# Kernel tuning notes

Hardware: AMD Instinct MI355X
Metric: run time of the kernel (lower is better)

## Reference

```python
import jax, jax.numpy as jnp
import numpy as np

THRESHOLD_IOU = 0.8  # forward default in the original module


def setup_inputs() -> dict:
    key = jax.random.key(0)
    k1, k2, k3, k4 = jax.random.split(key, 4)
    N = M = 16
    H = W = 768
    # Binary masks (the original zeroes pixels to 0.0 and tests >0 via torch.where)
    masks_a = (jax.random.uniform(k1, (N, H, W)) > 0.6).astype(jnp.float32)
    masks_b = (jax.random.uniform(k2, (M, H, W)) > 0.6).astype(jnp.float32)
    # Make a few masks identical across labels so the IoU>threshold (suppression)
    # branch is exercised, not just the partial-overlap zeroing branch.
    masks_b = masks_b.at[:4].set(masks_a[:4])
    scores_a = jax.random.uniform(k3, (N,))
    scores_b = jax.random.uniform(k4, (M,))
    return {"masks_a": masks_a, "masks_b": masks_b,
            "scores_a": scores_a, "scores_b": scores_b}


def _overlap_filter(masks_a, masks_b, scores_a, scores_b, thr):
    # Sequential pairwise IoU + overlap zeroing, faithful to the original
    # nested product(enumerate(masks), enumerate(other_masks)) loop order
    # (i outer, j inner), where each pair sees masks already modified by
    # earlier pairs. Pruning ("keep") is applied after the loop; here it is
    # represented with static shapes as keep flags + zeroed-out rows.
    N, H, W = masks_a.shape
    M = masks_b.shape[0]
    P = H * W
    A0 = masks_a.reshape(N, P)
    B0 = masks_b.reshape(M, P)

    def body(carry, k):
        A, B, fi, fj = carry
        i = k // M
        j = k % M
        a = A[i]  # [P]
        b = B[j]  # [P]
        abin = a > 0
        bbin = b > 0
        inter = abin & bbin
        inter_sum = jnp.sum(inter.astype(jnp.float32))
        union_sum = jnp.sum((abin | bbin).astype(jnp.float32))
        iou = inter_sum / jnp.maximum(union_sum, 1.0)
        a_wins = scores_a[i] > scores_b[j]
        suppress = iou > thr                 # mark whole loser mask for removal
        zero_case = (iou > 0) & ~suppress    # zero overlapped pixels of loser
        b_new = jnp.where(zero_case & a_wins & inter, 0.0, b)
        a_new = jnp.where(zero_case & (~a_wins) & inter, 0.0, a)
        A = A.at[i].set(a_new)
        B = B.at[j].set(b_new)
        fj = fj.at[j].set(fj[j] | (suppress & a_wins))
        fi = fi.at[i].set(fi[i] | (suppress & ~a_wins))
        return (A, B, fi, fj), None

    fi0 = jnp.zeros(N, dtype=bool)
    fj0 = jnp.zeros(M, dtype=bool)
    (A, B, fi, fj), _ = jax.lax.scan(body, (A0, B0, fi0, fj0), jnp.arange(N * M))
    keep_a = ~fi
    keep_b = ~fj
    A = jnp.where(keep_a[:, None], A, 0.0)
    B = jnp.where(keep_b[:, None], B, 0.0)
    return A.reshape(N, H, W), B.reshape(M, H, W), keep_a, keep_b


def reference(masks_a, masks_b, scores_a, scores_b):
    return _overlap_filter(masks_a, masks_b, scores_a, scores_b, THRESHOLD_IOU)
```

## Files before the change

### kernel.cpp

```cpp
#include <hip/hip_runtime.h>
#include <stdint.h>

#define NM 16
#define HW_P 589824
#define U8PM 9216
#define C4PM 4608
#define F4PM 147456
#define F4PT 2359296
#define PT 512
#define NG 8
#define EWG 64

typedef unsigned long long u64;
typedef float vf4 __attribute__((ext_vector_type(4)));


__device__ __forceinline__ unsigned aload(const unsigned* p) {
    return __hip_atomic_load(p, __ATOMIC_RELAXED, __HIP_MEMORY_SCOPE_AGENT);
}
__device__ __forceinline__ void astore(unsigned* p, unsigned v) {
    __hip_atomic_store(p, v, __ATOMIC_RELAXED, __HIP_MEMORY_SCOPE_AGENT);
}
__device__ __forceinline__ unsigned afadd(unsigned* p, unsigned v) {
    return __hip_atomic_fetch_add(p, v, __ATOMIC_RELAXED, __HIP_MEMORY_SCOPE_AGENT);
}
__device__ __forceinline__ u64 aload64(const u64* p) {
    return __hip_atomic_load(p, __ATOMIC_RELAXED, __HIP_MEMORY_SCOPE_AGENT);
}

__device__ __forceinline__ uint32_t spread4(uint32_t x) {
    uint32_t t = (x | (x << 12)) & 0x000F000Fu;
    t = (t | (t << 6)) & 0x03030303u;
    t = (t | (t << 3)) & 0x11111111u;
    return t;
}

__global__ __launch_bounds__(256) void binarize_kernel(
    const float* __restrict__ ma, const float* __restrict__ mb,
    uint32_t* __restrict__ bitsA, uint32_t* __restrict__ bitsB,
    uint4* __restrict__ meta4)
{
    if (blockIdx.x == 0) {
        uint4 z; z.x = z.y = z.z = z.w = 0u;
        meta4[threadIdx.x] = z;
    }
    int g = blockIdx.x * 256 + threadIdx.x;
    int tensor = (g >= F4PT);
    int lg = tensor ? (g - F4PT) : g;
    const float* src = tensor ? mb : ma;
    vf4 v = __builtin_nontemporal_load(((const vf4*)src) + lg);
    u64 q0 = __ballot(v.x > 0.0f);
    u64 q1 = __ballot(v.y > 0.0f);
    u64 q2 = __ballot(v.z > 0.0f);
    u64 q3 = __ballot(v.w > 0.0f);
    int lane = threadIdx.x & 63;
    if (lane < 8) {
        uint32_t wd = spread4((uint32_t)(q0 >> (8 * lane)) & 0xFFu)
                    | (spread4((uint32_t)(q1 >> (8 * lane)) & 0xFFu) << 1)
                    | (spread4((uint32_t)(q2 >> (8 * lane)) & 0xFFu) << 2)
                    | (spread4((uint32_t)(q3 >> (8 * lane)) & 0xFFu) << 3);
        uint32_t* bits = tensor ? bitsB : bitsA;
        bits[((lg & ~63) >> 3) + lane] = wd;
    }
}

__global__ __launch_bounds__(PT, 1) void pipeline_kernel(
    const float* __restrict__ sa, const float* __restrict__ sb,
    uint32_t* bitsA, uint32_t* bitsB, unsigned* meta, u64* msg)
{
    unsigned* cnt    = meta;
    unsigned* winner = meta + 8;
    int* flagsA      = (int*)(meta + 16);
    int* flagsB      = (int*)(meta + 32);
    unsigned* consF  = meta + 48;
    unsigned* prodF  = meta + 80;

    const int tid = threadIdx.x;
    const int wave = tid >> 6, lane = tid & 63;

    __shared__ int s_g;
    __shared__ int4 part[8];

    if (tid == 0) {
        int xcc;
        asm volatile("s_getreg_b32 %0, hwreg(HW_REG_XCC_ID)" : "=s"(xcc));
        xcc &= 7;
        unsigned slot = afadd(&cnt[xcc], 1u);
        int mine = -1;
        if (slot < NG) {
            if (slot == NG - 1) {
                unsigned exp = 0u;
                __hip_atomic_compare_exchange_strong(
                    winner, &exp, (unsigned)(xcc + 1),
                    __ATOMIC_RELAXED, __ATOMIC_RELAXED, __HIP_MEMORY_SCOPE_AGENT);
            }
            unsigned w;
            while (!(w = aload(winner))) __builtin_amdgcn_s_sleep(1);
            if (w == (unsigned)(xcc + 1)) mine = (int)slot;
        }
        s_g = mine;
    }
    __syncthreads();
    const int g = s_g;
    if (g < 0) return;

    const int c0 = 2 * g, c1 = 2 * g + 1;
    uint4* A4 = (uint4*)bitsA;
    uint4* B4 = (uint4*)bitsB;

    u64 b0[18], b1[18];

    int v0 = 0, v1 = 0;
#pragma unroll
    for (int w = 0; w < 9; ++w) {
        uint4 q0 = B4[(size_t)c0 * C4PM + tid + PT * w];
        uint4 q1 = B4[(size_t)c1 * C4PM + tid + PT * w];
        b0[2 * w] = ((u64)q0.y << 32) | q0.x; b0[2 * w + 1] = ((u64)q0.w << 32) | q0.z;
        b1[2 * w] = ((u64)q1.y << 32) | q1.x; b1[2 * w + 1] = ((u64)q1.w << 32) | q1.z;
        v0 += __popcll(b0[2 * w]) + __popcll(b0[2 * w + 1]);
        v1 += __popcll(b1[2 * w]) + __popcll(b1[2 * w + 1]);
    }
#pragma unroll
    for (int off = 32; off >= 1; off >>= 1) {
        v0 += __shfl_xor(v0, off); v1 += __shfl_xor(v1, off);
    }
    if (lane == 0) { int4 p; p.x = v0; p.y = v1; p.z = 0; p.w = 0; part[wave] = p; }
    __syncthreads();
    int pcb0 = 0, pcb1 = 0;
#pragma unroll
    for (int w = 0; w < 8; ++w) { pcb0 += part[w].x; pcb1 += part[w].y; }
    float sb0 = sb[c0], sb1 = sb[c1];
    int fb0 = 0, fb1 = 0;
    __syncthreads();

    for (int t = 0; t < NM; ++t) {
        int pca, fa;
        u64 a[18];

        if (g == 0) {
            pca = 0; fa = 0;
#pragma unroll
            for (int w = 0; w < 9; ++w) {
                uint4 q = A4[(size_t)t * C4PM + tid + PT * w];
                a[2 * w] = ((u64)q.y << 32) | q.x;
                a[2 * w + 1] = ((u64)q.w << 32) | q.z;
            }
        } else {
            const unsigned* fptr = &prodF[((g - 1) * 16 + t) * 4];
            unsigned v;
            do { v = aload(fptr); } while (!v);
            asm volatile("" ::: "memory");
            pca = (int)((v >> 1) & 0xFFFFFu);
            fa  = (int)((v >> 21) & 1u);
            const u64* slot_in = msg + (size_t)((g - 1) * 4 + (t & 3)) * U8PM;
#pragma unroll
            for (int w = 0; w < 9; ++w) {
                int base2 = 2 * tid + 1024 * w;
                a[2 * w]     = aload64(&slot_in[base2]);
                a[2 * w + 1] = aload64(&slot_in[base2 + 1]);
            }
        }

        int i0 = 0, i1 = 0, itr = 0, ipc = 0;
#pragma unroll
        for (int w = 0; w < 18; ++w) {
            u64 ab0 = a[w] & b0[w];
            i0 += __popcll(ab0);
            i1 += __popcll(a[w] & b1[w]);
            itr += __popcll(ab0 & b1[w]);
        }
        if (g == 0) {
#pragma unroll
            for (int w = 0; w < 18; ++w) ipc += __popcll(a[w]);
        }
#pragma unroll
        for (int off = 32; off >= 1; off >>= 1) {
            i0 += __shfl_xor(i0, off); i1 += __shfl_xor(i1, off);
            itr += __shfl_xor(itr, off); ipc += __shfl_xor(ipc, off);
        }
        if (lane == 0) {
            int4 p; p.x = i0; p.y = i1; p.z = itr; p.w = ipc; part[wave] = p;
        }
        __syncthreads();
        if (g > 0 && tid == 65)
            astore(&consF[(g - 1) * 4], (unsigned)(t + 1));
        int I0 = 0, I1 = 0, T = 0, PC = 0;
#pragma unroll
        for (int w = 0; w < 8; ++w) {
            int4 p = part[w];
            I0 += p.x; I1 += p.y; T += p.z; PC += p.w;
        }
        if (g == 0) pca = PC;

        float sai = sa[t];
        bool aupd = false;
        {
            int inter = I0;
            int uni = pca + pcb0 - inter;
            float iou = (float)inter / fmaxf((float)uni, 1.0f);
            bool aw = sai > sb0;
            if (iou > 0.8f) { if (aw) fb0 = 1; else fa = 1; }
            else if (inter > 0) {
                if (aw) {
                    pcb0 -= inter;
#pragma unroll
                    for (int w = 0; w < 18; ++w) b0[w] &= ~a[w];
                } else {
                    pca -= inter; aupd = true;
#pragma unroll
                    for (int w = 0; w < 18; ++w) a[w] &= ~b0[w];
                }
            }
        }
        {
            int inter = aupd ? (I1 - T) : I1;
            int uni = pca + pcb1 - inter;
            float iou = (float)inter / fmaxf((float)uni, 1.0f);
            bool aw = sai > sb1;
            if (iou > 0.8f) { if (aw) fb1 = 1; else fa = 1; }
            else if (inter > 0) {
                if (aw) {
                    pcb1 -= inter;
#pragma unroll
                    for (int w = 0; w < 18; ++w) b1[w] &= ~a[w];
                } else {
                    pca -= inter;
#pragma unroll
                    for (int w = 0; w < 18; ++w) a[w] &= ~b1[w];
                }
            }
        }

        if (g < NG - 1) {
            if (t >= 4) {
                const unsigned* cp = &consF[g * 4];
                while (aload(cp) < (unsigned)(t - 3)) {}
                asm volatile("" ::: "memory");
            }
            uint4* so = (uint4*)(msg + (size_t)(g * 4 + (t & 3)) * U8PM);
#pragma unroll
            for (int w = 0; w < 9; ++w) {
                uint4 q;
                q.x = (uint32_t)a[2 * w];     q.y = (uint32_t)(a[2 * w] >> 32);
                q.z = (uint32_t)a[2 * w + 1]; q.w = (uint32_t)(a[2 * w + 1] >> 32);
                so[tid + PT * w] = q;
            }
            __syncthreads();
            if (tid == 0)
                astore(&prodF[(g * 16 + t) * 4],
                       1u | ((unsigned)pca << 1) | ((unsigned)fa << 21));
        } else {
            uint4* Ar = A4 + (size_t)t * C4PM;
#pragma unroll
            for (int w = 0; w < 9; ++w) {
                uint4 q;
                q.x = (uint32_t)a[2 * w];     q.y = (uint32_t)(a[2 * w] >> 32);
                q.z = (uint32_t)a[2 * w + 1]; q.w = (uint32_t)(a[2 * w + 1] >> 32);
                Ar[tid + PT * w] = q;
            }
            if (tid == 0) flagsA[t] = fa;
            __syncthreads();
        }
    }

    uint4* Wc0 = B4 + (size_t)c0 * C4PM;
    uint4* Wc1 = B4 + (size_t)c1 * C4PM;
#pragma unroll
    for (int w = 0; w < 9; ++w) {
        uint4 q0, q1;
        q0.x = (uint32_t)b0[2 * w];     q0.y = (uint32_t)(b0[2 * w] >> 32);
        q0.z = (uint32_t)b0[2 * w + 1]; q0.w = (uint32_t)(b0[2 * w + 1] >> 32);
        q1.x = (uint32_t)b1[2 * w];     q1.y = (uint32_t)(b1[2 * w] >> 32);
        q1.z = (uint32_t)b1[2 * w + 1]; q1.w = (uint32_t)(b1[2 * w + 1] >> 32);
        Wc0[tid + PT * w] = q0;
        Wc1[tid + PT * w] = q1;
    }
    if (tid == 0) { flagsB[c0] = fb0; flagsB[c1] = fb1; }
}

__global__ __launch_bounds__(256) void expand_kernel(
    const uint32_t* __restrict__ bitsA, const uint32_t* __restrict__ bitsB,
    const int* __restrict__ meta, float* __restrict__ out)
{
    int g = blockIdx.x * 256 + threadIdx.x;
    int tensor = (g >= F4PT);
    int lg = tensor ? (g - F4PT) : g;
    const uint32_t* bits = tensor ? bitsB : bitsA;
    const int* flags = meta + (tensor ? 32 : 16);
    int m = lg / F4PM;
    bool keep = (flags[m] == 0);
    uint32_t wd = keep ? bits[lg >> 3] : 0u;
    int sh = (lg & 7) * 4;
    vf4 o;
    o.x = ((wd >> (sh + 0)) & 1u) ? 1.0f : 0.0f;
    o.y = ((wd >> (sh + 1)) & 1u) ? 1.0f : 0.0f;
    o.z = ((wd >> (sh + 2)) & 1u) ? 1.0f : 0.0f;
    o.w = ((wd >> (sh + 3)) & 1u) ? 1.0f : 0.0f;
    __builtin_nontemporal_store(o, ((vf4*)out) + g);
    if (g < 2 * NM) {
        out[(size_t)2 * NM * HW_P + g] = meta[16 + g] ? 0.0f : 1.0f;
    }
}

extern "C" void kernel_launch(void* const* d_in, const int* in_sizes, int n_in,
                              void* d_out, int out_size, void* d_ws, size_t ws_size,
                              hipStream_t stream)
{
    const float* ma = (const float*)d_in[0];
    const float* mb = (const float*)d_in[1];
    const float* sa = (const float*)d_in[2];
    const float* sb = (const float*)d_in[3];
    float* out = (float*)d_out;
    char* ws = (char*)d_ws;

    uint32_t* bitsA = (uint32_t*)(ws);
    uint32_t* bitsB = (uint32_t*)(ws + 1179648);
    unsigned* meta  = (unsigned*)(ws + 2359296);
    u64* msg        = (u64*)(ws + 2363392);

    binarize_kernel<<<18432, 256, 0, stream>>>(ma, mb, bitsA, bitsB,
                                               (uint4*)meta);
    pipeline_kernel<<<EWG, PT, 0, stream>>>(sa, sb, bitsA, bitsB, meta, msg);
    expand_kernel<<<18432, 256, 0, stream>>>(bitsA, bitsB, (const int*)meta, out);
}
```

Before: 226.8 us.

## Split each pipeline stage across two workgroups exchanging half-mask partial counts

Each of the eight pipeline stages is now split over two workgroups, each handling half of the pixel range, so the launch needs 16 co-resident workgroups on one XCC instead of 8. Partner workgroups swap their partial intersection and popcount sums every step through agent-scope atomic slots tagged with the step number, and the message buffers now carry half-masks. This halves per-workgroup register data and per-step memory traffic to shorten the serial critical path, but it adds a cross-workgroup handshake on every step and more spin-waiting.

```diff
diff --git a/kernel.cpp b/kernel.cpp
--- a/kernel.cpp
+++ b/kernel.cpp
@@ -4,12 +4,13 @@
 #define NM 16
 #define HW_P 589824
 #define U8PM 9216
-#define C4PM 4608
+#define U8PH 4608
 #define F4PM 147456
 #define F4PT 2359296
 #define PT 512
 #define NG 8
-#define EWG 64
+#define NW 16
+#define EWG 128
 
 typedef unsigned long long u64;
 typedef float vf4 __attribute__((ext_vector_type(4)));
@@ -26,6 +27,9 @@
 }
 __device__ __forceinline__ u64 aload64(const u64* p) {
     return __hip_atomic_load(p, __ATOMIC_RELAXED, __HIP_MEMORY_SCOPE_AGENT);
+}
+__device__ __forceinline__ void astore64(u64* p, u64 v) {
+    __hip_atomic_store(p, v, __ATOMIC_RELAXED, __HIP_MEMORY_SCOPE_AGENT);
 }
 
 __device__ __forceinline__ uint32_t spread4(uint32_t x) {
@@ -43,6 +47,7 @@
     if (blockIdx.x == 0) {
         uint4 z; z.x = z.y = z.z = z.w = 0u;
         meta4[threadIdx.x] = z;
+        meta4[threadIdx.x + 256] = z;
     }
     int g = blockIdx.x * 256 + threadIdx.x;
     int tensor = (g >= F4PT);
@@ -73,12 +78,13 @@
     int* flagsA      = (int*)(meta + 16);
     int* flagsB      = (int*)(meta + 32);
     unsigned* consF  = meta + 48;
-    unsigned* prodF  = meta + 80;
+    unsigned* prodF  = meta + 112;
+    u64* xchg        = (u64*)(meta + 1024);
 
     const int tid = threadIdx.x;
     const int wave = tid >> 6, lane = tid & 63;
 
-    __shared__ int s_g;
+    __shared__ int s_slot;
     __shared__ int4 part[8];
 
     if (tid == 0) {
@@ -87,8 +93,8 @@
         xcc &= 7;
         unsigned slot = afadd(&cnt[xcc], 1u);
         int mine = -1;
-        if (slot < NG) {
-            if (slot == NG - 1) {
+        if (slot < NW) {
+            if (slot == NW - 1) {
                 unsigned exp = 0u;
                 __hip_atomic_compare_exchange_strong(
                     winner, &exp, (unsigned)(xcc + 1),
@@ -98,72 +104,103 @@
             while (!(w = aload(winner))) __builtin_amdgcn_s_sleep(1);
             if (w == (unsigned)(xcc + 1)) mine = (int)slot;
         }
-        s_g = mine;
+        s_slot = mine;
     }
     __syncthreads();
-    const int g = s_g;
-    if (g < 0) return;
+    const int sl = s_slot;
+    if (sl < 0) return;
+    const int g = sl >> 1, h = sl & 1;
+    const int ch = g * 2 + h;
+    const int inch = (g - 1) * 2 + h;
+
+    u64* A8 = (u64*)bitsA;
+    u64* B8 = (u64*)bitsB;
+
+    auto load9 = [&](const u64* base, u64* dst) {
+        const uint4* b4 = (const uint4*)base;
+#pragma unroll
+        for (int w = 0; w < 4; ++w) {
+            uint4 q = b4[tid + PT * w];
+            dst[2 * w]     = ((u64)q.y << 32) | q.x;
+            dst[2 * w + 1] = ((u64)q.w << 32) | q.z;
+        }
+        dst[8] = base[4096 + tid];
+    };
+    auto load9_agent = [&](const u64* base, u64* dst) {
+#pragma unroll
+        for (int w = 0; w < 4; ++w) {
+            int i2 = 2 * tid + 1024 * w;
+            dst[2 * w]     = aload64(&base[i2]);
+            dst[2 * w + 1] = aload64(&base[i2 + 1]);
+        }
+        dst[8] = aload64(&base[4096 + tid]);
+    };
+    auto store9 = [&](u64* base, const u64* src) {
+        uint4* b4 = (uint4*)base;
+#pragma unroll
+        for (int w = 0; w < 4; ++w) {
+            uint4 q;
+            q.x = (uint32_t)src[2 * w];     q.y = (uint32_t)(src[2 * w] >> 32);
+            q.z = (uint32_t)src[2 * w + 1]; q.w = (uint32_t)(src[2 * w + 1] >> 32);
+            b4[tid + PT * w] = q;
+        }
+        base[4096 + tid] = src[8];
+    };
 
     const int c0 = 2 * g, c1 = 2 * g + 1;
-    uint4* A4 = (uint4*)bitsA;
-    uint4* B4 = (uint4*)bitsB;
-
-    u64 b0[18], b1[18];
-
+    u64 b0[9], b1[9];
+    load9(B8 + (size_t)c0 * U8PM + (size_t)h * U8PH, b0);
+    load9(B8 + (size_t)c1 * U8PM + (size_t)h * U8PH, b1);
     int v0 = 0, v1 = 0;
 #pragma unroll
-    for (int w = 0; w < 9; ++w) {
-        uint4 q0 = B4[(size_t)c0 * C4PM + tid + PT * w];
-        uint4 q1 = B4[(size_t)c1 * C4PM + tid + PT * w];
-        b0[2 * w] = ((u64)q0.y << 32) | q0.x; b0[2 * w + 1] = ((u64)q0.w << 32) | q0.z;
-        b1[2 * w] = ((u64)q1.y << 32) | q1.x; b1[2 * w + 1] = ((u64)q1.w << 32) | q1.z;
-        v0 += __popcll(b0[2 * w]) + __popcll(b0[2 * w + 1]);
-        v1 += __popcll(b1[2 * w]) + __popcll(b1[2 * w + 1]);
-    }
+    for (int w = 0; w < 9; ++w) { v0 += __popcll(b0[w]); v1 += __popcll(b1[w]); }
 #pragma unroll
     for (int off = 32; off >= 1; off >>= 1) {
         v0 += __shfl_xor(v0, off); v1 += __shfl_xor(v1, off);
     }
     if (lane == 0) { int4 p; p.x = v0; p.y = v1; p.z = 0; p.w = 0; part[wave] = p; }
     __syncthreads();
-    int pcb0 = 0, pcb1 = 0;
-#pragma unroll
-    for (int w = 0; w < 8; ++w) { pcb0 += part[w].x; pcb1 += part[w].y; }
+    int pcb0h = 0, pcb1h = 0;
+#pragma unroll
+    for (int w = 0; w < 8; ++w) { pcb0h += part[w].x; pcb1h += part[w].y; }
+    __syncthreads();
+
+    {
+        u64* myx = xchg + (size_t)(ch * 2 + 1) * 2;
+        if (tid == 0)
+            astore64(&myx[0], (u64)pcb0h | ((u64)pcb1h << 20) | (1ull << 40));
+    }
+    int pcb0, pcb1;
+    {
+        const u64* px = xchg + (size_t)((g * 2 + (1 - h)) * 2 + 1) * 2;
+        u64 x0;
+        do { x0 = aload64(&px[0]); } while ((unsigned)(x0 >> 40) != 1u);
+        pcb0 = pcb0h + (int)(x0 & 0xFFFFF);
+        pcb1 = pcb1h + (int)((x0 >> 20) & 0xFFFFF);
+    }
     float sb0 = sb[c0], sb1 = sb[c1];
     int fb0 = 0, fb1 = 0;
-    __syncthreads();
 
     for (int t = 0; t < NM; ++t) {
         int pca, fa;
-        u64 a[18];
+        u64 a[9];
 
         if (g == 0) {
+            load9(A8 + (size_t)t * U8PM + (size_t)h * U8PH, a);
             pca = 0; fa = 0;
-#pragma unroll
-            for (int w = 0; w < 9; ++w) {
-                uint4 q = A4[(size_t)t * C4PM + tid + PT * w];
-                a[2 * w] = ((u64)q.y << 32) | q.x;
-                a[2 * w + 1] = ((u64)q.w << 32) | q.z;
-            }
         } else {
-            const unsigned* fptr = &prodF[((g - 1) * 16 + t) * 4];
+            const unsigned* fptr = &prodF[(inch * 16 + t) * 4];
             unsigned v;
             do { v = aload(fptr); } while (!v);
             asm volatile("" ::: "memory");
             pca = (int)((v >> 1) & 0xFFFFFu);
             fa  = (int)((v >> 21) & 1u);
-            const u64* slot_in = msg + (size_t)((g - 1) * 4 + (t & 3)) * U8PM;
-#pragma unroll
-            for (int w = 0; w < 9; ++w) {
-                int base2 = 2 * tid + 1024 * w;
-                a[2 * w]     = aload64(&slot_in[base2]);
-                a[2 * w + 1] = aload64(&slot_in[base2 + 1]);
-            }
+            load9_agent(msg + (size_t)(inch * 4 + (t & 3)) * U8PH, a);
         }
 
         int i0 = 0, i1 = 0, itr = 0, ipc = 0;
 #pragma unroll
-        for (int w = 0; w < 18; ++w) {
+        for (int w = 0; w < 9; ++w) {
             u64 ab0 = a[w] & b0[w];
             i0 += __popcll(ab0);
             i1 += __popcll(a[w] & b1[w]);
@@ -171,7 +208,7 @@
         }
         if (g == 0) {
 #pragma unroll
-            for (int w = 0; w < 18; ++w) ipc += __popcll(a[w]);
+            for (int w = 0; w < 9; ++w) ipc += __popcll(a[w]);
         }
 #pragma unroll
         for (int off = 32; off >= 1; off >>= 1) {
@@ -183,12 +220,32 @@
         }
         __syncthreads();
         if (g > 0 && tid == 65)
-            astore(&consF[(g - 1) * 4], (unsigned)(t + 1));
-        int I0 = 0, I1 = 0, T = 0, PC = 0;
+            astore(&consF[inch * 4], (unsigned)(t + 1));
+        int I0h = 0, I1h = 0, Th = 0, PCh = 0;
 #pragma unroll
         for (int w = 0; w < 8; ++w) {
             int4 p = part[w];
-            I0 += p.x; I1 += p.y; T += p.z; PC += p.w;
+            I0h += p.x; I1h += p.y; Th += p.z; PCh += p.w;
+        }
+
+        unsigned tg = (unsigned)(t + 2);
+        {
+            u64* myx = xchg + (size_t)(ch * 2 + (t & 1)) * 2;
+            if (tid == 0) {
+                astore64(&myx[0], (u64)I0h | ((u64)I1h << 20) | ((u64)tg << 40));
+                astore64(&myx[1], (u64)Th  | ((u64)PCh << 20) | ((u64)tg << 40));
+            }
+        }
+        int I0, I1, T, PC;
+        {
+            const u64* px = xchg + (size_t)((g * 2 + (1 - h)) * 2 + (t & 1)) * 2;
+            u64 x0, x1;
+            do { x0 = aload64(&px[0]); } while ((unsigned)(x0 >> 40) != tg);
+            do { x1 = aload64(&px[1]); } while ((unsigned)(x1 >> 40) != tg);
+            I0 = I0h + (int)(x0 & 0xFFFFF);
+            I1 = I1h + (int)((x0 >> 20) & 0xFFFFF);
+            T  = Th  + (int)(x1 & 0xFFFFF);
+            PC = PCh + (int)((x1 >> 20) & 0xFFFFF);
         }
         if (g == 0) pca = PC;
 
@@ -204,11 +261,11 @@
                 if (aw) {
                     pcb0 -= inter;
 #pragma unroll
-                    for (int w = 0; w < 18; ++w) b0[w] &= ~a[w];
+                    for (int w = 0; w < 9; ++w) b0[w] &= ~a[w];
                 } else {
                     pca -= inter; aupd = true;
 #pragma unroll
-                    for (int w = 0; w < 18; ++w) a[w] &= ~b0[w];
+                    for (int w = 0; w < 9; ++w) a[w] &= ~b0[w];
                 }
             }
         }
@@ -222,60 +279,36 @@
                 if (aw) {
                     pcb1 -= inter;
 #pragma unroll
-                    for (int w = 0; w < 18; ++w) b1[w] &= ~a[w];
+                    for (int w = 0; w < 9; ++w) b1[w] &= ~a[w];
                 } else {
                     pca -= inter;
 #pragma unroll
-                    for (int w = 0; w < 18; ++w) a[w] &= ~b1[w];
+                    for (int w = 0; w < 9; ++w) a[w] &= ~b1[w];
                 }
             }
         }
 
         if (g < NG - 1) {
             if (t >= 4) {
-                const unsigned* cp = &consF[g * 4];
+                const unsigned* cp = &consF[ch * 4];
                 while (aload(cp) < (unsigned)(t - 3)) {}
                 asm volatile("" ::: "memory");
             }
-            uint4* so = (uint4*)(msg + (size_t)(g * 4 + (t & 3)) * U8PM);
-#pragma unroll
-            for (int w = 0; w < 9; ++w) {
-                uint4 q;
-                q.x = (uint32_t)a[2 * w];     q.y = (uint32_t)(a[2 * w] >> 32);
-                q.z = (uint32_t)a[2 * w + 1]; q.w = (uint32_t)(a[2 * w + 1] >> 32);
-                so[tid + PT * w] = q;
-            }
+            store9(msg + (size_t)(ch * 4 + (t & 3)) * U8PH, a);
             __syncthreads();
             if (tid == 0)
-                astore(&prodF[(g * 16 + t) * 4],
+                astore(&prodF[(ch * 16 + t) * 4],
                        1u | ((unsigned)pca << 1) | ((unsigned)fa << 21));
         } else {
-            uint4* Ar = A4 + (size_t)t * C4PM;
-#pragma unroll
-            for (int w = 0; w < 9; ++w) {
-                uint4 q;
-                q.x = (uint32_t)a[2 * w];     q.y = (uint32_t)(a[2 * w] >> 32);
-                q.z = (uint32_t)a[2 * w + 1]; q.w = (uint32_t)(a[2 * w + 1] >> 32);
-                Ar[tid + PT * w] = q;
-            }
-            if (tid == 0) flagsA[t] = fa;
+            store9(A8 + (size_t)t * U8PM + (size_t)h * U8PH, a);
+            if (h == 0 && tid == 0) flagsA[t] = fa;
             __syncthreads();
         }
     }
 
-    uint4* Wc0 = B4 + (size_t)c0 * C4PM;
-    uint4* Wc1 = B4 + (size_t)c1 * C4PM;
-#pragma unroll
-    for (int w = 0; w < 9; ++w) {
-        uint4 q0, q1;
-        q0.x = (uint32_t)b0[2 * w];     q0.y = (uint32_t)(b0[2 * w] >> 32);
-        q0.z = (uint32_t)b0[2 * w + 1]; q0.w = (uint32_t)(b0[2 * w + 1] >> 32);
-        q1.x = (uint32_t)b1[2 * w];     q1.y = (uint32_t)(b1[2 * w] >> 32);
-        q1.z = (uint32_t)b1[2 * w + 1]; q1.w = (uint32_t)(b1[2 * w + 1] >> 32);
-        Wc0[tid + PT * w] = q0;
-        Wc1[tid + PT * w] = q1;
-    }
-    if (tid == 0) { flagsB[c0] = fb0; flagsB[c1] = fb1; }
+    store9(B8 + (size_t)c0 * U8PM + (size_t)h * U8PH, b0);
+    store9(B8 + (size_t)c1 * U8PM + (size_t)h * U8PH, b1);
+    if (h == 0 && tid == 0) { flagsB[c0] = fb0; flagsB[c1] = fb1; }
 }
 
 __global__ __launch_bounds__(256) void expand_kernel(
@@ -316,7 +349,7 @@
     uint32_t* bitsA = (uint32_t*)(ws);
     uint32_t* bitsB = (uint32_t*)(ws + 1179648);
     unsigned* meta  = (unsigned*)(ws + 2359296);
-    u64* msg        = (u64*)(ws + 2363392);
+    u64* msg        = (u64*)(ws + 2367488);
 
     binarize_kernel<<<18432, 256, 0, stream>>>(ma, mb, bitsA, bitsB,
                                                (uint4*)meta);
```

New measurement: 227.7 us. About the same (+0.4%).
